# Performance work log

Hardware: AMD Instinct MI355X
Metric: run time of the kernel (lower is better)

The kernel has to match this reference:

```python
import jax, jax.numpy as jnp
import numpy as np

S = 4096          # seq_len (longformer-large-4096)
H = 1024          # hidden_size
FF = 3072         # ffnn_size (hardcoded)
G = 100           # number of gold mentions
MAX_SPAN = 30     # max_span_length
TOP_LAMBDA = 0.2
LN_EPS = 1e-5
MASK_VAL = 10000.0


def setup_inputs() -> dict:
    key = jax.random.key(0)
    ks = jax.random.split(key, 16)
    sc = 0.02
    sequence_output = jax.random.normal(ks[0], (1, S, H), jnp.float32)
    attention_mask = jnp.ones((1, S), jnp.int32)
    # valid gold spans: 1 <= start <= end < start + MAX_SPAN (so torch's >0 filter keeps all)
    gs = jax.random.randint(ks[1], (G,), 1, S - MAX_SPAN)
    gl = jax.random.randint(ks[2], (G,), 0, MAX_SPAN)
    gold_mentions = jnp.stack([gs, gs + gl], axis=1).astype(jnp.int32)  # [G, 2]
    inp = {
        'sequence_output': sequence_output,
        'attention_mask': attention_mask,
        'gold_mentions': gold_mentions,
        # start_mention_mlp
        'W_sm': jax.random.normal(ks[3], (H, FF), jnp.float32) * sc,
        'b_sm': jnp.zeros((FF,), jnp.float32),
        'g_sm': jnp.ones((FF,), jnp.float32),
        'beta_sm': jnp.zeros((FF,), jnp.float32),
        # end_mention_mlp
        'W_em': jax.random.normal(ks[4], (H, FF), jnp.float32) * sc,
        'b_em': jnp.zeros((FF,), jnp.float32),
        'g_em': jnp.ones((FF,), jnp.float32),
        'beta_em': jnp.zeros((FF,), jnp.float32),
        # classifiers
        'w_start': jax.random.normal(ks[5], (FF,), jnp.float32) * sc,
        'b_start': jnp.zeros((), jnp.float32),
        'w_end': jax.random.normal(ks[6], (FF,), jnp.float32) * sc,
        'b_end': jnp.zeros((), jnp.float32),
        'W_s2e': jax.random.normal(ks[7], (FF, FF), jnp.float32) * sc,
        'b_s2e': jnp.zeros((FF,), jnp.float32),
    }
    return inp


def _fcl(x, W, b, g, beta):
    # dense -> gelu (exact) -> layernorm (dropout is identity in eval)
    h = jax.nn.gelu(x @ W + b, approximate=False)
    mu = jnp.mean(h, axis=-1, keepdims=True)
    var = jnp.mean(jnp.square(h - mu), axis=-1, keepdims=True)
    return (h - mu) * jax.lax.rsqrt(var + LN_EPS) * g + beta


def _forward(sequence_output, attention_mask, gold_mentions,
             W_sm, b_sm, g_sm, beta_sm, W_em, b_em, g_em, beta_em,
             w_start, b_start, w_end, b_end, W_s2e, b_s2e):
    start_reps = _fcl(sequence_output, W_sm, b_sm, g_sm, beta_sm)  # [1,S,FF]
    end_reps = _fcl(sequence_output, W_em, b_em, g_em, beta_em)    # [1,S,FF]

    start_logits = jnp.einsum('bsf,f->bs', start_reps, w_start) + b_start  # [1,S]
    end_logits = jnp.einsum('bsf,f->bs', end_reps, w_end) + b_end          # [1,S]
    temp = start_reps @ W_s2e + b_s2e                                      # [1,S,FF]
    joint = jnp.einsum('bsf,btf->bst', temp, end_reps)                     # [1,S,S]
    mention_logits = joint + start_logits[:, :, None] + end_logits[:, None, :]

    # span mask: start <= end < start + MAX_SPAN (triu(0) then tril(MAX_SPAN-1))
    i = jnp.arange(S)
    mention_mask = ((i[:, None] <= i[None, :]) & (i[None, :] < i[:, None] + MAX_SPAN)
                    ).astype(jnp.float32)[None]  # [1,S,S]
    mention_logits = jnp.clip(mention_logits + (1.0 - mention_mask) * (-MASK_VAL),
                              -MASK_VAL, MASK_VAL)

    # top-k pruning; attention_mask is full so k is static: int(S * 0.2)
    max_k = int(S * TOP_LAMBDA)  # 819
    _, topk_1d = jax.lax.top_k(mention_logits.reshape(1, -1), max_k)  # [1,max_k]
    sorted_idx = jnp.sort(topk_1d, axis=-1)
    topk_start_ids = sorted_idx // S
    topk_end_ids = sorted_idx % S
    span_mask = jnp.ones((1, max_k), jnp.float32)

    # losses
    probs = jax.nn.sigmoid(mention_logits)  # [1,S,S]
    gstart = gold_mentions[:, 0]
    gend = gold_mentions[:, 1]
    gold_probs = probs[0, gstart, gend]
    # torch BCE clamps log at -100
    cost_gold = -jnp.mean(jnp.maximum(jnp.log(gold_probs), -100.0))
    junk = probs.at[0, gstart, gend].set(0.0)
    log1mp = jnp.maximum(jnp.log(1.0 - junk), -100.0)
    cost_junk = -jnp.sum(jnp.where(mention_mask == 1.0, log1mp, 0.0)) / jnp.sum(mention_mask)
    cost_is_mention = (cost_gold + cost_junk)[None]  # [1]

    return topk_start_ids, topk_end_ids, span_mask, sequence_output, cost_is_mention


def reference(sequence_output, attention_mask, gold_mentions,
              W_sm, b_sm, g_sm, beta_sm, W_em, b_em, g_em, beta_em,
              w_start, b_start, w_end, b_end, W_s2e, b_s2e):
    return _forward(sequence_output, attention_mask, gold_mentions,
                    W_sm, b_sm, g_sm, beta_sm, W_em, b_em, g_em, beta_em,
                    w_start, b_start, w_end, b_end, W_s2e, b_s2e)
```

## Files before the change

### kernel.cpp

```cpp
#include <hip/hip_runtime.h>
#include <math.h>

#define S 4096
#define H 1024
#define FF 3072
#define G 100
#define MAXSPAN 30
#define MAXK 819
#define NBAND (S * MAXSPAN)
#define BAND_COUNT 122445.0

#define O_START 0
#define O_END   819
#define O_MASK  1638
#define O_SEQ   2457
#define O_COST  (2457 + S * H)

typedef __bf16 bf16x8 __attribute__((ext_vector_type(8)));
typedef float f32x16 __attribute__((ext_vector_type(16)));


__device__ __forceinline__ float block_reduce_256(float x, volatile float* red) {
  #pragma unroll
  for (int off = 32; off > 0; off >>= 1) x += __shfl_down(x, off, 64);
  int wid = threadIdx.x >> 6;
  int lane = threadIdx.x & 63;
  __syncthreads();
  if (lane == 0) red[wid] = x;
  __syncthreads();
  return red[0] + red[1] + red[2] + red[3];
}

__device__ __forceinline__ float block_reduce_1024(float x, volatile float* red) {
  #pragma unroll
  for (int off = 32; off > 0; off >>= 1) x += __shfl_down(x, off, 64);
  int wid = threadIdx.x >> 6;
  int lane = threadIdx.x & 63;
  __syncthreads();
  if (lane == 0) red[wid] = x;
  __syncthreads();
  float s = 0.f;
  #pragma unroll
  for (int q = 0; q < 16; q++) s += red[q];
  return s;
}

__device__ __forceinline__ unsigned f2key(float f) {
  unsigned b = __float_as_uint(f);
  return (b & 0x80000000u) ? ~b : (b | 0x80000000u);
}

__device__ __forceinline__ unsigned short bf16_rne(float x) {
  unsigned u = __float_as_uint(x);
  unsigned r = ((u >> 16) & 1u) + 0x7FFFu;
  return (unsigned short)((u + r) >> 16);
}

__device__ __forceinline__ void split2(float x, unsigned short& h, unsigned short& l) {
  h = bf16_rne(x);
  float hf = __uint_as_float(((unsigned)h) << 16);
  l = bf16_rne(x - hf);
}

__device__ __forceinline__ void gld16(const void* g, void* l) {
  __builtin_amdgcn_global_load_lds(
      (const __attribute__((address_space(1))) unsigned int*)g,
      (__attribute__((address_space(3))) unsigned int*)l, 16, 0, 0);
}


__device__ __forceinline__ void pack_a_body(const float* __restrict__ A,
                                            float* __restrict__ Aout,
                                            unsigned short* __restrict__ hi,
                                            unsigned short* __restrict__ lo,
                                            int K, int bx, int by) {
  __shared__ float tile[32][33];
  const int t = threadIdx.x;
  const int tx = t & 31, ty8 = t >> 5;
  const int k0 = bx * 32, r0 = by * 32;
  #pragma unroll
  for (int r = ty8; r < 32; r += 8) {
    float v = A[(size_t)(r0 + r) * K + k0 + tx];
    tile[r][tx] = v;
    if (Aout) Aout[(size_t)(r0 + r) * K + k0 + tx] = v;
  }
  __syncthreads();
  if (t < 128) {
    const int kql = t >> 5;
    const int rl = t & 31;
    unsigned short h8[8], l8[8];
    #pragma unroll
    for (int s = 0; s < 8; s++) split2(tile[rl][kql * 8 + s], h8[s], l8[s]);
    const size_t panel = (size_t)(r0 >> 7);
    const int rloc = (r0 & 127) + rl;
    const size_t off = panel * (size_t)(128 * K) + (size_t)(k0 / 8 + kql) * 1024 + (size_t)rloc * 8;
    *(uint4*)(hi + off) = *(const uint4*)h8;
    *(uint4*)(lo + off) = *(const uint4*)l8;
  }
}

__device__ __forceinline__ void pack_ln_a_body(const float* __restrict__ A,
                                               const float* __restrict__ mu,
                                               const float* __restrict__ rstd,
                                               const float* __restrict__ g,
                                               const float* __restrict__ beta,
                                               unsigned short* __restrict__ hi,
                                               unsigned short* __restrict__ lo,
                                               int K, int bx, int by) {
  __shared__ float tile[32][33];
  const int t = threadIdx.x;
  const int tx = t & 31, ty8 = t >> 5;
  const int k0 = bx * 32, r0 = by * 32;
  #pragma unroll
  for (int r = ty8; r < 32; r += 8)
    tile[r][tx] = A[(size_t)(r0 + r) * K + k0 + tx];
  __syncthreads();
  if (t < 128) {
    const int kql = t >> 5;
    const int rl = t & 31;
    const int row = r0 + rl;
    const float m = mu[row], rs = rstd[row];
    float4 g0 = *(const float4*)(g + k0 + kql * 8);
    float4 g1 = *(const float4*)(g + k0 + kql * 8 + 4);
    float4 b0 = *(const float4*)(beta + k0 + kql * 8);
    float4 b1 = *(const float4*)(beta + k0 + kql * 8 + 4);
    float gv[8] = {g0.x, g0.y, g0.z, g0.w, g1.x, g1.y, g1.z, g1.w};
    float bv[8] = {b0.x, b0.y, b0.z, b0.w, b1.x, b1.y, b1.z, b1.w};
    unsigned short h8[8], l8[8];
    #pragma unroll
    for (int s = 0; s < 8; s++) {
      float v = (tile[rl][kql * 8 + s] - m) * rs * gv[s] + bv[s];
      split2(v, h8[s], l8[s]);
    }
    const size_t panel = (size_t)(r0 >> 7);
    const int rloc = (r0 & 127) + rl;
    const size_t off = panel * (size_t)(128 * K) + (size_t)(k0 / 8 + kql) * 1024 + (size_t)rloc * 8;
    *(uint4*)(hi + off) = *(const uint4*)h8;
    *(uint4*)(lo + off) = *(const uint4*)l8;
  }
}

__device__ __forceinline__ void pack_bt_body(const float* __restrict__ W,
                                             unsigned short* __restrict__ hi,
                                             unsigned short* __restrict__ lo,
                                             int K, int N, int bx, int by) {
  __shared__ float tile[32][33];
  const int t = threadIdx.x;
  const int tx = t & 31, ty8 = t >> 5;
  const int k0 = bx * 32, n0 = by * 32;
  #pragma unroll
  for (int r = ty8; r < 32; r += 8)
    tile[r][tx] = W[(size_t)(k0 + r) * N + n0 + tx];
  __syncthreads();
  if (t < 128) {
    const int kql = t >> 5;
    const int nl = t & 31;
    unsigned short h8[8], l8[8];
    #pragma unroll
    for (int s = 0; s < 8; s++) split2(tile[kql * 8 + s][nl], h8[s], l8[s]);
    const size_t panel = (size_t)(n0 >> 7);
    const int nloc = (n0 & 127) + nl;
    const size_t off = panel * (size_t)(128 * K) + (size_t)(k0 / 8 + kql) * 1024 + (size_t)nloc * 8;
    *(uint4*)(hi + off) = *(const uint4*)h8;
    *(uint4*)(lo + off) = *(const uint4*)l8;
  }
}

__global__ __launch_bounds__(256) void pack_head_kernel(const float* __restrict__ seq,
                                                        float* __restrict__ seq_out,
                                                        unsigned short* __restrict__ sh,
                                                        unsigned short* __restrict__ sl,
                                                        const float* __restrict__ W1,
                                                        const float* __restrict__ W2,
                                                        unsigned short* __restrict__ w1h,
                                                        unsigned short* __restrict__ w1l,
                                                        unsigned short* __restrict__ w2h,
                                                        unsigned short* __restrict__ w2l) {
  const int y = blockIdx.y;
  if (y < 128)      pack_a_body(seq, seq_out, sh, sl, H, blockIdx.x, y);
  else if (y < 224) pack_bt_body(W1, w1h, w1l, H, FF, blockIdx.x, y - 128);
  else              pack_bt_body(W2, w2h, w2l, H, FF, blockIdx.x, y - 224);
}

__global__ __launch_bounds__(256) void pack_mid_kernel(const float* __restrict__ bufS,
                                                       const float* __restrict__ muS,
                                                       const float* __restrict__ rstdS,
                                                       const float* __restrict__ g,
                                                       const float* __restrict__ beta,
                                                       unsigned short* __restrict__ ahi,
                                                       unsigned short* __restrict__ alo,
                                                       const float* __restrict__ Ws2e,
                                                       unsigned short* __restrict__ wbh,
                                                       unsigned short* __restrict__ wbl) {
  const int y = blockIdx.y;
  if (y < 128) pack_ln_a_body(bufS, muS, rstdS, g, beta, ahi, alo, FF, blockIdx.x, y);
  else         pack_bt_body(Ws2e, wbh, wbl, FF, FF, blockIdx.x, y - 128);
}

#define SLOTB 28672
#define A_STR 8192
#define B_BASE 16384
#define B_STR 6144

template <int EPI>
__device__ __forceinline__ void gemm8_body(const char* __restrict__ cAh, const char* __restrict__ cAl,
                                           const char* __restrict__ cBh, const char* __restrict__ cBl,
                                           const float* __restrict__ bias,
                                           float* __restrict__ C,
                                           int bm, int bn, int N, int K,
                                           char* smem) {
  const int tid = threadIdx.x;
  const int lane = tid & 63;
  const int wid = __builtin_amdgcn_readfirstlane(tid >> 6);
  const int wm = wid >> 1, wn = wid & 1;
  const int khalf = lane >> 5;
  const int r31 = lane & 31;
  const size_t PS = (size_t)256 * (size_t)K;

  const char* lsrc[4];
  int ldst[4];
  #pragma unroll
  for (int i = 0; i < 4; i++) { lsrc[i] = cAh; ldst[i] = 0; }
  if (wid < 7) {
    #pragma unroll
    for (int i = 0; i < 4; i++) {
      int q = wid * 4 + i;
      if (q < 16) {
        int str = q >> 3, r = q & 7, kql = r >> 2, u = r & 3;
        lsrc[i] = (str ? cAl : cAh) + (size_t)((bm >> 7) + (u >> 1)) * PS
                + (size_t)(kql * 2048 + (u & 1) * 1024 + lane * 16);
        ldst[i] = str * A_STR + kql * 4096 + u * 1024;
      } else {
        int qq = q - 16;
        int str = qq / 6, r = qq % 6, kql = r / 3, v = r % 3;
        int gcol = bn + 64 * v;
        lsrc[i] = (str ? cBl : cBh) + (size_t)(gcol >> 7) * PS
                + (size_t)(kql * 2048 + ((gcol >> 6) & 1) * 1024 + lane * 16);
        ldst[i] = B_BASE + str * B_STR + kql * 3072 + v * 1024;
      }
    }
  }

  const int aoff = khalf * 4096 + (wm * 64 + r31) * 16;
  const int boff = B_BASE + khalf * 3072 + (wn * 96 + r31) * 16;

  f32x16 acc[2][3];
  #pragma unroll
  for (int mt = 0; mt < 2; mt++)
    #pragma unroll
    for (int nt = 0; nt < 3; nt++)
      #pragma unroll
      for (int r = 0; r < 16; r++) acc[mt][nt][r] = 0.0f;

  auto stage = [&](int h) {
    if (wid < 7) {
      char* sb = smem + (h & 3) * SLOTB;
      const size_t ko = (size_t)h * 4096;
      #pragma unroll
      for (int i = 0; i < 4; i++) gld16(lsrc[i] + ko, sb + ldst[i]);
    }
  };

  const int NH = K >> 4;

  stage(0); stage(1); stage(2);
  asm volatile("s_waitcnt vmcnt(8)" ::: "memory");
  __builtin_amdgcn_s_barrier();

  for (int p = 0; p < NH; ++p) {
    const char* sm = smem + (p & 3) * SLOTB;
    if (p + 3 < NH) stage(p + 3);
    bf16x8 ah[2], al[2], bh[3], bl[3];
    #pragma unroll
    for (int mt = 0; mt < 2; mt++) ah[mt] = *(const bf16x8*)(sm + aoff + mt * 512);
    #pragma unroll
    for (int nt = 0; nt < 3; nt++) bh[nt] = *(const bf16x8*)(sm + boff + nt * 512);
    #pragma unroll
    for (int mt = 0; mt < 2; mt++) al[mt] = *(const bf16x8*)(sm + A_STR + aoff + mt * 512);
    #pragma unroll
    for (int nt = 0; nt < 3; nt++) bl[nt] = *(const bf16x8*)(sm + B_STR + boff + nt * 512);
    __builtin_amdgcn_s_setprio(1);
    #pragma unroll
    for (int mt = 0; mt < 2; mt++)
      #pragma unroll
      for (int nt = 0; nt < 3; nt++)
        acc[mt][nt] = __builtin_amdgcn_mfma_f32_32x32x16_bf16(ah[mt], bh[nt], acc[mt][nt], 0, 0, 0);
    #pragma unroll
    for (int mt = 0; mt < 2; mt++)
      #pragma unroll
      for (int nt = 0; nt < 3; nt++)
        acc[mt][nt] = __builtin_amdgcn_mfma_f32_32x32x16_bf16(al[mt], bh[nt], acc[mt][nt], 0, 0, 0);
    #pragma unroll
    for (int mt = 0; mt < 2; mt++)
      #pragma unroll
      for (int nt = 0; nt < 3; nt++)
        acc[mt][nt] = __builtin_amdgcn_mfma_f32_32x32x16_bf16(ah[mt], bl[nt], acc[mt][nt], 0, 0, 0);
    __builtin_amdgcn_s_setprio(0);
    if (p + 4 < NH)       { asm volatile("s_waitcnt vmcnt(8)" ::: "memory"); }
    else if (p + 3 == NH) { asm volatile("s_waitcnt vmcnt(4)" ::: "memory"); }
    else if (p + 2 == NH) { asm volatile("s_waitcnt vmcnt(0)" ::: "memory"); }
    if (p + 1 < NH) __builtin_amdgcn_s_barrier();
  }

  #pragma unroll
  for (int mt = 0; mt < 2; mt++) {
    #pragma unroll
    for (int nt = 0; nt < 3; nt++) {
      const int colg = bn + wn * 96 + nt * 32 + r31;
      const float bb = bias[colg];
      #pragma unroll
      for (int reg = 0; reg < 16; reg++) {
        const int rowl = (reg & 3) + 8 * (reg >> 2) + 4 * khalf;
        const int rowg = bm + wm * 64 + mt * 32 + rowl;
        float v = acc[mt][nt][reg] + bb;
        if (EPI == 1) v = 0.5f * v * (1.0f + erff(v * 0.70710678118654752f));
        C[(size_t)rowg * N + colg] = v;
      }
    }
  }
}

__device__ __forceinline__ void grid_swizzle_16x16(int& bx, int& by) {
  const int lin = blockIdx.y * 16 + blockIdx.x;
  const int X = lin & 7, c = lin >> 3;
  bx = (X & 3) * 4 + (c & 3);
  by = (X >> 2) * 8 + (c >> 2);
}

__global__ __launch_bounds__(512) void gemm_mfma_kernel(const unsigned short* __restrict__ Ahi,
                                                        const unsigned short* __restrict__ Alo,
                                                        const unsigned short* __restrict__ Bhi,
                                                        const unsigned short* __restrict__ Blo,
                                                        const float* __restrict__ bias,
                                                        float* __restrict__ C,
                                                        int N, int K) {
  __shared__ __align__(16) char smem[4 * SLOTB];
  int bx, by;
  grid_swizzle_16x16(bx, by);
  gemm8_body<0>((const char*)Ahi, (const char*)Alo,
                (const char*)Bhi, (const char*)Blo,
                bias, C, by * 256, bx * 192, N, K, smem);
}

__global__ __launch_bounds__(512) void gemm_mfma_dual_kernel(const unsigned short* __restrict__ Ahi,
                                                             const unsigned short* __restrict__ Alo,
                                                             const unsigned short* __restrict__ B1hi,
                                                             const unsigned short* __restrict__ B1lo,
                                                             const unsigned short* __restrict__ B2hi,
                                                             const unsigned short* __restrict__ B2lo,
                                                             const float* __restrict__ bias1,
                                                             const float* __restrict__ bias2,
                                                             float* __restrict__ C1,
                                                             float* __restrict__ C2,
                                                             int N, int K) {
  __shared__ __align__(16) char smem[4 * SLOTB];
  const int zb = blockIdx.z;
  const unsigned short* Bhi = zb ? B2hi : B1hi;
  const unsigned short* Blo = zb ? B2lo : B1lo;
  const float* bias = zb ? bias2 : bias1;
  float* C = zb ? C2 : C1;
  int bx, by;
  grid_swizzle_16x16(bx, by);
  gemm8_body<1>((const char*)Ahi, (const char*)Alo,
                (const char*)Bhi, (const char*)Blo,
                bias, C, by * 256, bx * 192, N, K, smem);
}


__global__ __launch_bounds__(256) void ln_stats_kernel(const float* __restrict__ HbS,
                                                       const float* __restrict__ HbE,
                                                       const float* __restrict__ gS,
                                                       const float* __restrict__ betaS,
                                                       const float* __restrict__ wS,
                                                       const float* __restrict__ bS,
                                                       const float* __restrict__ gE,
                                                       const float* __restrict__ betaE,
                                                       const float* __restrict__ wE,
                                                       const float* __restrict__ bE,
                                                       float* __restrict__ slog,
                                                       float* __restrict__ elog,
                                                       float* __restrict__ muS,
                                                       float* __restrict__ rstdS,
                                                       float* __restrict__ muE,
                                                       float* __restrict__ rstdE) {
  __shared__ float red[4];
  const int row = blockIdx.x, tid = threadIdx.x;
  const int br = blockIdx.y;
  const float* Hb = br ? HbE : HbS;
  const float* g = br ? gE : gS;
  const float* beta = br ? betaE : betaS;
  const float* w = br ? wE : wS;
  const float* bsc = br ? bE : bS;
  const float* h = Hb + (size_t)row * FF;

  float4 v[3];
  float s = 0.0f;
  #pragma unroll
  for (int t = 0; t < 3; t++) {
    v[t] = *(const float4*)(h + tid * 4 + t * 1024);
    s += v[t].x + v[t].y + v[t].z + v[t].w;
  }
  float mu = block_reduce_256(s, red) * (1.0f / (float)FF);

  float s2 = 0.0f;
  #pragma unroll
  for (int t = 0; t < 3; t++) {
    float dx = v[t].x - mu, dy = v[t].y - mu, dz = v[t].z - mu, dw = v[t].w - mu;
    s2 += dx * dx + dy * dy + dz * dz + dw * dw;
  }
  float var = block_reduce_256(s2, red) * (1.0f / (float)FF);
  float rstd = rsqrtf(var + 1e-5f);

  float dot = 0.0f;
  #pragma unroll
  for (int t = 0; t < 3; t++) {
    int idx = tid * 4 + t * 1024;
    float4 gv = *(const float4*)(g + idx);
    float4 bv = *(const float4*)(beta + idx);
    float4 wv = *(const float4*)(w + idx);
    float rx = (v[t].x - mu) * rstd * gv.x + bv.x;
    float ry = (v[t].y - mu) * rstd * gv.y + bv.y;
    float rz = (v[t].z - mu) * rstd * gv.z + bv.z;
    float rw = (v[t].w - mu) * rstd * gv.w + bv.w;
    dot += rx * wv.x + ry * wv.y + rz * wv.z + rw * wv.w;
  }
  float dt = block_reduce_256(dot, red);
  if (tid == 0) {
    if (br) { elog[row] = dt + bsc[0]; muE[row] = mu; rstdE[row] = rstd; }
    else    { slog[row] = dt + bsc[0]; muS[row] = mu; rstdS[row] = rstd; }
  }
}


__global__ __launch_bounds__(256) void band_joint_kernel(const float* __restrict__ T,
                                                         const float* __restrict__ Eraw,
                                                         const float* __restrict__ muE,
                                                         const float* __restrict__ rstdE,
                                                         const float* __restrict__ gE,
                                                         const float* __restrict__ betaE,
                                                         const float* __restrict__ sl,
                                                         const float* __restrict__ el,
                                                         float* __restrict__ band,
                                                         double* __restrict__ jacc,
                                                         unsigned* __restrict__ hist16) {
  __shared__ float Elds[45][260];
  __shared__ float red[4];
  const int t = threadIdx.x;
  const int bx = blockIdx.x;
  const int sbx = (bx & 7) * 32 + (bx >> 3);
  const int i0 = sbx * 16;
  const int r_l = t >> 4, c = t & 15;

  float accd[MAXSPAN];
  #pragma unroll
  for (int d = 0; d < MAXSPAN; d++) accd[d] = 0.0f;

  for (int k0 = 0; k0 < FF; k0 += 256) {
    const float* trow = T + (size_t)(i0 + r_l) * FF + k0 + c * 16;
    float4 tv0 = *(const float4*)(trow + 0);
    float4 tv1 = *(const float4*)(trow + 4);
    float4 tv2 = *(const float4*)(trow + 8);
    float4 tv3 = *(const float4*)(trow + 12);
    __syncthreads();
    for (int rr = t >> 6; rr < 45; rr += 4) {
      int gr = i0 + rr;
      int cc = (t & 63) * 4;
      float4 rv = {0.f, 0.f, 0.f, 0.f};
      if (gr < S) {
        float4 ev = *(const float4*)(Eraw + (size_t)gr * FF + k0 + cc);
        float m = muE[gr], rs = rstdE[gr];
        float4 gv = *(const float4*)(gE + k0 + cc);
        float4 bv = *(const float4*)(betaE + k0 + cc);
        rv.x = (ev.x - m) * rs * gv.x + bv.x;
        rv.y = (ev.y - m) * rs * gv.y + bv.y;
        rv.z = (ev.z - m) * rs * gv.z + bv.z;
        rv.w = (ev.w - m) * rs * gv.w + bv.w;
      }
      *(float4*)&Elds[rr][cc] = rv;
    }
    __syncthreads();
    #pragma unroll
    for (int d = 0; d < MAXSPAN; d++) {
      const float* er = &Elds[r_l + d][c * 16];
      float4 e0 = *(const float4*)(er + 0);
      float4 e1 = *(const float4*)(er + 4);
      float4 e2 = *(const float4*)(er + 8);
      float4 e3 = *(const float4*)(er + 12);
      accd[d] += tv0.x * e0.x + tv0.y * e0.y + tv0.z * e0.z + tv0.w * e0.w
               + tv1.x * e1.x + tv1.y * e1.y + tv1.z * e1.z + tv1.w * e1.w
               + tv2.x * e2.x + tv2.y * e2.y + tv2.z * e2.z + tv2.w * e2.w
               + tv3.x * e3.x + tv3.y * e3.y + tv3.z * e3.z + tv3.w * e3.w;
    }
  }

  const int i = i0 + r_l;
  const float my_sl = sl[i];
  float jsum = 0.0f;
  #pragma unroll
  for (int d = 0; d < MAXSPAN; d++) {
    float v = accd[d];
    v += __shfl_down(v, 8, 16);
    v += __shfl_down(v, 4, 16);
    v += __shfl_down(v, 2, 16);
    v += __shfl_down(v, 1, 16);
    if (c == 0) {
      int j = i + d;
      if (j < S) {
        float vv = v + my_sl + el[j];
        vv = fminf(fmaxf(vv, -10000.0f), 10000.0f);
        band[i * MAXSPAN + d] = vv;
        atomicAdd(&hist16[f2key(vv) >> 16], 1u);
        float p = 1.0f / (1.0f + expf(-vv));
        jsum += fmaxf(logf(1.0f - p), -100.0f);
      } else {
        band[i * MAXSPAN + d] = -1e30f;
      }
    }
  }
  float tot = block_reduce_256(jsum, red);
  if (t == 0) atomicAdd(jacc, (double)tot);
}


__global__ __launch_bounds__(1024) void topk_finalize_kernel(const float* __restrict__ band,
                                                             const int* __restrict__ gold,
                                                             const double* __restrict__ jacc,
                                                             const unsigned* __restrict__ hist16,
                                                             float* __restrict__ out) {
  __shared__ int csum[1024];
  __shared__ unsigned sh_T16;
  __shared__ int sh_remk;
  __shared__ int sh_chunk, sh_above;
  __shared__ int idxbuf[1024];
  __shared__ unsigned tkey[256];
  __shared__ int tidx[256];
  __shared__ int cnt_gt, cnt_eq;
  __shared__ int sb[1024];
  __shared__ int gcell[G];
  __shared__ float redf[16];
  const int tid = threadIdx.x;

  int s = 0;
  #pragma unroll 8
  for (int q = 0; q < 64; q++) s += (int)hist16[tid * 64 + q];
  csum[tid] = s;
  __syncthreads();
  for (int off = 1; off < 1024; off <<= 1) {
    int v = (tid + off < 1024) ? csum[tid + off] : 0;
    __syncthreads();
    csum[tid] += v;
    __syncthreads();
  }
  {
    int nxt = (tid < 1023) ? csum[tid + 1] : 0;
    if (csum[tid] >= MAXK && nxt < MAXK) { sh_chunk = tid; sh_above = nxt; }
  }
  __syncthreads();
  if (tid == 0) {
    int cum = sh_above;
    int b = sh_chunk * 64 + 63;
    for (;; b--) {
      int h = (int)hist16[b];
      if (cum + h >= MAXK || b == sh_chunk * 64) { sh_T16 = (unsigned)b; sh_remk = MAXK - cum; break; }
      cum += h;
    }
  }
  __syncthreads();
  const unsigned T16 = sh_T16;
  int remk = sh_remk;

  if (tid == 0) { cnt_gt = 0; cnt_eq = 0; }
  __syncthreads();
  for (int e = tid; e < NBAND; e += 1024) {
    unsigned key = f2key(band[e]);
    unsigned k16 = key >> 16;
    if (k16 >= T16) {
      int i = e / MAXSPAN, d = e - i * MAXSPAN;
      int fi = i * S + i + d;
      if (k16 > T16) {
        int p = atomicAdd(&cnt_gt, 1);
        if (p < 1024) idxbuf[p] = fi;
      } else {
        int p = atomicAdd(&cnt_eq, 1);
        if (p < 256) { tkey[p] = key; tidx[p] = fi; }
      }
    }
  }
  __syncthreads();
  if (tid == 0) {
    int ngt = cnt_gt < 1024 ? cnt_gt : 1024;
    int ne = cnt_eq < 256 ? cnt_eq : 256;
    for (int a2 = 1; a2 < ne; a2++) {
      unsigned kv = tkey[a2]; int iv = tidx[a2];
      int b2 = a2 - 1;
      while (b2 >= 0 && (tkey[b2] < kv || (tkey[b2] == kv && tidx[b2] > iv))) {
        tkey[b2 + 1] = tkey[b2]; tidx[b2 + 1] = tidx[b2]; b2--;
      }
      tkey[b2 + 1] = kv; tidx[b2 + 1] = iv;
    }
    int take = remk < ne ? remk : ne;
    for (int q = 0; q < take; q++)
      if (ngt + q < 1024) idxbuf[ngt + q] = tidx[q];
  }
  __syncthreads();

  sb[tid] = (tid < MAXK) ? idxbuf[tid] : 0x7FFFFFFF;
  __syncthreads();
  for (int ksz = 2; ksz <= 1024; ksz <<= 1) {
    for (int jj = ksz >> 1; jj > 0; jj >>= 1) {
      int ixj = tid ^ jj;
      if (ixj > tid) {
        int a2 = sb[tid], b2 = sb[ixj];
        bool up = ((tid & ksz) == 0);
        if (up ? (a2 > b2) : (a2 < b2)) { sb[tid] = b2; sb[ixj] = a2; }
      }
      __syncthreads();
    }
  }
  if (tid < MAXK) {
    int fi = sb[tid];
    out[O_START + tid] = (float)(fi >> 12);
    out[O_END + tid]   = (float)(fi & 4095);
    out[O_MASK + tid]  = 1.0f;
  }

  if (tid < G) {
    int gs = gold[2 * tid], ge = gold[2 * tid + 1];
    gcell[tid] = gs * MAXSPAN + (ge - gs);
  }
  __syncthreads();
  float tg = 0.0f, tj = 0.0f;
  if (tid < G) {
    int cell = gcell[tid];
    float x = band[cell];
    float p = 1.0f / (1.0f + expf(-x));
    tg = fmaxf(logf(p), -100.0f);
    bool first = true;
    for (int q = 0; q < tid; q++)
      if (gcell[q] == cell) { first = false; break; }
    if (first) tj = fmaxf(logf(1.0f - p), -100.0f);
  }
  float sg = block_reduce_1024(tg, redf);
  float sj = block_reduce_1024(tj, redf);
  if (tid == 0) {
    double junk = *jacc - (double)sj;
    double cost = -((double)sg / (double)G) - (junk / BAND_COUNT);
    out[O_COST] = (float)cost;
  }
}


extern "C" void kernel_launch(void* const* d_in, const int* in_sizes, int n_in,
                              void* d_out, int out_size, void* d_ws, size_t ws_size,
                              hipStream_t stream) {
  (void)in_sizes; (void)n_in; (void)out_size; (void)ws_size;
  const float* seq    = (const float*)d_in[0];
  const int*   gold   = (const int*)d_in[2];
  const float* W_sm   = (const float*)d_in[3];
  const float* b_sm   = (const float*)d_in[4];
  const float* g_sm   = (const float*)d_in[5];
  const float* be_sm  = (const float*)d_in[6];
  const float* W_em   = (const float*)d_in[7];
  const float* b_em   = (const float*)d_in[8];
  const float* g_em   = (const float*)d_in[9];
  const float* be_em  = (const float*)d_in[10];
  const float* w_st   = (const float*)d_in[11];
  const float* b_st   = (const float*)d_in[12];
  const float* w_en   = (const float*)d_in[13];
  const float* b_en   = (const float*)d_in[14];
  const float* W_s2e  = (const float*)d_in[15];
  const float* b_s2e  = (const float*)d_in[16];
  float* out = (float*)d_out;
  char* ws = (char*)d_ws;

  const size_t SZ_REP = (size_t)S * FF * 4;
  float*  bufS = (float*)(ws);
  float*  bufE = (float*)(ws + SZ_REP);
  float*  bufT = (float*)(ws + 2 * SZ_REP);
  char* R3 = ws + 3 * SZ_REP;
  unsigned short* seqhi = (unsigned short*)R3;
  unsigned short* seqlo = (unsigned short*)(R3 + (size_t)S * H * 2);
  unsigned short* a3hi  = (unsigned short*)R3;
  unsigned short* a3lo  = (unsigned short*)(R3 + (size_t)S * FF * 2);
  char* R4 = ws + 4 * SZ_REP;
  const size_t SZ_W12 = (size_t)H * FF * 2;
  unsigned short* wb1hi = (unsigned short*)R4;
  unsigned short* wb1lo = (unsigned short*)(R4 + SZ_W12);
  unsigned short* wb2hi = (unsigned short*)(R4 + 2 * SZ_W12);
  unsigned short* wb2lo = (unsigned short*)(R4 + 3 * SZ_W12);
  unsigned short* wbhi = (unsigned short*)R4;
  unsigned short* wblo = (unsigned short*)(R4 + (size_t)FF * FF * 2);
  char* R5 = R4 + 2 * (size_t)FF * FF * 2;
  float*    band   = (float*)R5;
  unsigned* hist16 = (unsigned*)(R5 + (size_t)NBAND * 4);
  double*   jacc   = (double*)(R5 + (size_t)NBAND * 4 + 262144);
  float*    slog   = (float*)(R5 + (size_t)NBAND * 4 + 262144 + 64);
  float*  elog  = slog + S;
  float*  muS   = elog + S;
  float*  rstdS = muS + S;
  float*  muE   = rstdS + S;
  float*  rstdE = muE + S;

  hipMemsetAsync(hist16, 0, 262144 + 64 + 8, stream);

  dim3 gg(16, 16);
  dim3 gg2(16, 16, 2);

  pack_head_kernel<<<dim3(32, 320), 256, 0, stream>>>(seq, out + O_SEQ, seqhi, seqlo,
                                                      W_sm, W_em, wb1hi, wb1lo, wb2hi, wb2lo);
  gemm_mfma_dual_kernel<<<gg2, 512, 0, stream>>>(seqhi, seqlo, wb1hi, wb1lo, wb2hi, wb2lo,
                                                 b_sm, b_em, bufS, bufE, FF, H);
  ln_stats_kernel<<<dim3(S, 2), 256, 0, stream>>>(bufS, bufE, g_sm, be_sm, w_st, b_st,
                                                  g_em, be_em, w_en, b_en,
                                                  slog, elog, muS, rstdS, muE, rstdE);
  pack_mid_kernel<<<dim3(96, 224), 256, 0, stream>>>(bufS, muS, rstdS, g_sm, be_sm,
                                                     a3hi, a3lo, W_s2e, wbhi, wblo);
  gemm_mfma_kernel<<<gg, 512, 0, stream>>>(a3hi, a3lo, wbhi, wblo, b_s2e, bufT, FF, FF);

  band_joint_kernel<<<S / 16, 256, 0, stream>>>(bufT, bufE, muE, rstdE, g_em, be_em,
                                                slog, elog, band, jacc, hist16);

  topk_finalize_kernel<<<1, 1024, 0, stream>>>(band, gold, jacc, hist16, out);
}
```

Measured before the change: 780.2 us.

## Shrink GEMM tile to 128x192 with 4 warps and triple-buffered LDS

Result: no change. 784.6 us (+0.6%).

```diff
diff --git a/kernel.cpp b/kernel.cpp
--- a/kernel.cpp
+++ b/kernel.cpp
@@ -197,9 +197,9 @@
   else         pack_bt_body(Ws2e, wbh, wbl, FF, FF, blockIdx.x, y - 128);
 }
 
-#define SLOTB 28672
-#define A_STR 8192
-#define B_BASE 16384
+#define SLOTB 20480
+#define A_STR 4096
+#define B_BASE 8192
 #define B_STR 6144
 
 template <int EPI>
@@ -217,31 +217,27 @@
   const int r31 = lane & 31;
   const size_t PS = (size_t)256 * (size_t)K;
 
-  const char* lsrc[4];
-  int ldst[4];
-  #pragma unroll
-  for (int i = 0; i < 4; i++) { lsrc[i] = cAh; ldst[i] = 0; }
-  if (wid < 7) {
-    #pragma unroll
-    for (int i = 0; i < 4; i++) {
-      int q = wid * 4 + i;
-      if (q < 16) {
-        int str = q >> 3, r = q & 7, kql = r >> 2, u = r & 3;
-        lsrc[i] = (str ? cAl : cAh) + (size_t)((bm >> 7) + (u >> 1)) * PS
-                + (size_t)(kql * 2048 + (u & 1) * 1024 + lane * 16);
-        ldst[i] = str * A_STR + kql * 4096 + u * 1024;
-      } else {
-        int qq = q - 16;
-        int str = qq / 6, r = qq % 6, kql = r / 3, v = r % 3;
-        int gcol = bn + 64 * v;
-        lsrc[i] = (str ? cBl : cBh) + (size_t)(gcol >> 7) * PS
-                + (size_t)(kql * 2048 + ((gcol >> 6) & 1) * 1024 + lane * 16);
-        ldst[i] = B_BASE + str * B_STR + kql * 3072 + v * 1024;
-      }
-    }
-  }
-
-  const int aoff = khalf * 4096 + (wm * 64 + r31) * 16;
+  const char* lsrc[5];
+  int ldst[5];
+  #pragma unroll
+  for (int i = 0; i < 5; i++) {
+    int q = wid * 5 + i;
+    if (q < 8) {
+      int str = q >> 2, r = q & 3, kql = r >> 1, u = r & 1;
+      lsrc[i] = (str ? cAl : cAh) + (size_t)(bm >> 7) * PS
+              + (size_t)(kql * 2048 + u * 1024 + lane * 16);
+      ldst[i] = str * A_STR + kql * 2048 + u * 1024;
+    } else {
+      int qq = q - 8;
+      int str = qq / 6, rr = qq % 6, kql = rr / 3, v = rr % 3;
+      int gcol = bn + 64 * v;
+      lsrc[i] = (str ? cBl : cBh) + (size_t)(gcol >> 7) * PS
+              + (size_t)(kql * 2048 + ((gcol >> 6) & 1) * 1024 + lane * 16);
+      ldst[i] = B_BASE + str * B_STR + kql * 3072 + v * 1024;
+    }
+  }
+
+  const int aoff = khalf * 2048 + (wm * 64 + r31) * 16;
   const int boff = B_BASE + khalf * 3072 + (wn * 96 + r31) * 16;
 
   f32x16 acc[2][3];
@@ -253,23 +249,21 @@
       for (int r = 0; r < 16; r++) acc[mt][nt][r] = 0.0f;
 
   auto stage = [&](int h) {
-    if (wid < 7) {
-      char* sb = smem + (h & 3) * SLOTB;
-      const size_t ko = (size_t)h * 4096;
-      #pragma unroll
-      for (int i = 0; i < 4; i++) gld16(lsrc[i] + ko, sb + ldst[i]);
-    }
+    char* sb = smem + (h % 3) * SLOTB;
+    const size_t ko = (size_t)h * 4096;
+    #pragma unroll
+    for (int i = 0; i < 5; i++) gld16(lsrc[i] + ko, sb + ldst[i]);
   };
 
   const int NH = K >> 4;
 
-  stage(0); stage(1); stage(2);
-  asm volatile("s_waitcnt vmcnt(8)" ::: "memory");
+  stage(0); stage(1);
+  asm volatile("s_waitcnt vmcnt(5)" ::: "memory");
   __builtin_amdgcn_s_barrier();
 
   for (int p = 0; p < NH; ++p) {
-    const char* sm = smem + (p & 3) * SLOTB;
-    if (p + 3 < NH) stage(p + 3);
+    const char* sm = smem + (p % 3) * SLOTB;
+    if (p + 2 < NH) stage(p + 2);
     bf16x8 ah[2], al[2], bh[3], bl[3];
     #pragma unroll
     for (int mt = 0; mt < 2; mt++) ah[mt] = *(const bf16x8*)(sm + aoff + mt * 512);
@@ -283,22 +277,14 @@
     #pragma unroll
     for (int mt = 0; mt < 2; mt++)
       #pragma unroll
-      for (int nt = 0; nt < 3; nt++)
+      for (int nt = 0; nt < 3; nt++) {
         acc[mt][nt] = __builtin_amdgcn_mfma_f32_32x32x16_bf16(ah[mt], bh[nt], acc[mt][nt], 0, 0, 0);
-    #pragma unroll
-    for (int mt = 0; mt < 2; mt++)
-      #pragma unroll
-      for (int nt = 0; nt < 3; nt++)
         acc[mt][nt] = __builtin_amdgcn_mfma_f32_32x32x16_bf16(al[mt], bh[nt], acc[mt][nt], 0, 0, 0);
-    #pragma unroll
-    for (int mt = 0; mt < 2; mt++)
-      #pragma unroll
-      for (int nt = 0; nt < 3; nt++)
         acc[mt][nt] = __builtin_amdgcn_mfma_f32_32x32x16_bf16(ah[mt], bl[nt], acc[mt][nt], 0, 0, 0);
+      }
     __builtin_amdgcn_s_setprio(0);
-    if (p + 4 < NH)       { asm volatile("s_waitcnt vmcnt(8)" ::: "memory"); }
-    else if (p + 3 == NH) { asm volatile("s_waitcnt vmcnt(4)" ::: "memory"); }
-    else if (p + 2 == NH) { asm volatile("s_waitcnt vmcnt(0)" ::: "memory"); }
+    if (p + 2 < NH)      { asm volatile("s_waitcnt vmcnt(5)" ::: "memory"); }
+    else if (p + 1 < NH) { asm volatile("s_waitcnt vmcnt(0)" ::: "memory"); }
     if (p + 1 < NH) __builtin_amdgcn_s_barrier();
   }
 
@@ -320,29 +306,29 @@
   }
 }
 
-__device__ __forceinline__ void grid_swizzle_16x16(int& bx, int& by) {
+__device__ __forceinline__ void grid_swizzle_16x32(int& bx, int& by) {
   const int lin = blockIdx.y * 16 + blockIdx.x;
   const int X = lin & 7, c = lin >> 3;
   bx = (X & 3) * 4 + (c & 3);
-  by = (X >> 2) * 8 + (c >> 2);
-}
-
-__global__ __launch_bounds__(512) void gemm_mfma_kernel(const unsigned short* __restrict__ Ahi,
+  by = (X >> 2) * 16 + (c >> 2);
+}
+
+__global__ __launch_bounds__(256) void gemm_mfma_kernel(const unsigned short* __restrict__ Ahi,
                                                         const unsigned short* __restrict__ Alo,
                                                         const unsigned short* __restrict__ Bhi,
                                                         const unsigned short* __restrict__ Blo,
                                                         const float* __restrict__ bias,
                                                         float* __restrict__ C,
                                                         int N, int K) {
-  __shared__ __align__(16) char smem[4 * SLOTB];
+  __shared__ __align__(16) char smem[3 * SLOTB];
   int bx, by;
-  grid_swizzle_16x16(bx, by);
+  grid_swizzle_16x32(bx, by);
   gemm8_body<0>((const char*)Ahi, (const char*)Alo,
                 (const char*)Bhi, (const char*)Blo,
-                bias, C, by * 256, bx * 192, N, K, smem);
-}
-
-__global__ __launch_bounds__(512) void gemm_mfma_dual_kernel(const unsigned short* __restrict__ Ahi,
+                bias, C, by * 128, bx * 192, N, K, smem);
+}
+
+__global__ __launch_bounds__(256) void gemm_mfma_dual_kernel(const unsigned short* __restrict__ Ahi,
                                                              const unsigned short* __restrict__ Alo,
                                                              const unsigned short* __restrict__ B1hi,
                                                              const unsigned short* __restrict__ B1lo,
@@ -353,17 +339,17 @@
                                                              float* __restrict__ C1,
                                                              float* __restrict__ C2,
                                                              int N, int K) {
-  __shared__ __align__(16) char smem[4 * SLOTB];
+  __shared__ __align__(16) char smem[3 * SLOTB];
   const int zb = blockIdx.z;
   const unsigned short* Bhi = zb ? B2hi : B1hi;
   const unsigned short* Blo = zb ? B2lo : B1lo;
   const float* bias = zb ? bias2 : bias1;
   float* C = zb ? C2 : C1;
   int bx, by;
-  grid_swizzle_16x16(bx, by);
+  grid_swizzle_16x32(bx, by);
   gemm8_body<1>((const char*)Ahi, (const char*)Alo,
                 (const char*)Bhi, (const char*)Blo,
-                bias, C, by * 256, bx * 192, N, K, smem);
+                bias, C, by * 128, bx * 192, N, K, smem);
 }
 
 
@@ -703,19 +689,19 @@
 
   hipMemsetAsync(hist16, 0, 262144 + 64 + 8, stream);
 
-  dim3 gg(16, 16);
-  dim3 gg2(16, 16, 2);
+  dim3 gg(16, 32);
+  dim3 gg2(16, 32, 2);
 
   pack_head_kernel<<<dim3(32, 320), 256, 0, stream>>>(seq, out + O_SEQ, seqhi, seqlo,
                                                       W_sm, W_em, wb1hi, wb1lo, wb2hi, wb2lo);
-  gemm_mfma_dual_kernel<<<gg2, 512, 0, stream>>>(seqhi, seqlo, wb1hi, wb1lo, wb2hi, wb2lo,
+  gemm_mfma_dual_kernel<<<gg2, 256, 0, stream>>>(seqhi, seqlo, wb1hi, wb1lo, wb2hi, wb2lo,
                                                  b_sm, b_em, bufS, bufE, FF, H);
   ln_stats_kernel<<<dim3(S, 2), 256, 0, stream>>>(bufS, bufE, g_sm, be_sm, w_st, b_st,
                                                   g_em, be_em, w_en, b_en,
                                                   slog, elog, muS, rstdS, muE, rstdE);
   pack_mid_kernel<<<dim3(96, 224), 256, 0, stream>>>(bufS, muS, rstdS, g_sm, be_sm,
                                                      a3hi, a3lo, W_s2e, wbhi, wblo);
-  gemm_mfma_kernel<<<gg, 512, 0, stream>>>(a3hi, a3lo, wbhi, wblo, b_s2e, bufT, FF, FF);
+  gemm_mfma_kernel<<<gg, 256, 0, stream>>>(a3hi, a3lo, wbhi, wblo, b_s2e, bufT, FF, FF);
 
   band_joint_kernel<<<S / 16, 256, 0, stream>>>(bufT, bufE, muE, rstdE, g_em, be_em,
                                                 slog, elog, band, jacc, hist16);
```
